# Kernel tuning notes

Measured on AMD Instinct MI355X. Metric: run time of the kernel, lower is better.

Reference implementation:

```python
import jax, jax.numpy as jnp
import numpy as np

BETA = 1.0
ALPHA = 0.5
M, D, B = 65536, 256, 512


def setup_inputs() -> dict:
    key = jax.random.key(0)
    k1, k2, k3 = jax.random.split(key, 3)
    v = jax.random.normal(k1, (B, D), dtype=jnp.float32)
    mask = jax.random.uniform(k2, (B, D), dtype=jnp.float32)
    memories = jax.random.normal(k3, (M, D), dtype=jnp.float32)
    return {"v": v, "mask": mask, "memories": memories}


def reference(v, mask, memories):
    # logits[m, b] = -beta/2 * ||memories[m] - v[b]||^2
    # expanded via ||a-b||^2 = ||a||^2 - 2 a.b + ||b||^2 (same math, no [M,D,B] tensor)
    mem_sq = jnp.sum(memories * memories, axis=1, keepdims=True)      # [M, 1]
    v_sq = jnp.sum(v * v, axis=1)[None, :]                            # [1, B]
    cross = jnp.einsum('md,bd->mb', memories, v)                      # [M, B]
    logits = -0.5 * BETA * (mem_sq - 2.0 * cross + v_sq)              # [M, B]
    # w = exp(logits) / sum_m exp(logits): stable softmax over memories
    w = jax.nn.softmax(logits, axis=0)                                # [M, B]
    # update[b, d] = sum_m w[m,b] * (memories[m,d] - v[b,d])
    #            = (w^T @ memories)[b,d] - v[b,d]
    update = jnp.einsum('mb,md->bd', w, memories) - v                 # [B, D]
    out = v + ALPHA * update * mask                                   # [B, D]
    return out
```

## Files before the change

kernel.cpp:

```cpp
#include <hip/hip_runtime.h>
#include <hip/hip_bf16.h>


#define D_DIM 256
#define B_DIM 512
#define M_TOT 65536
#define NSPLIT 64
#define CHUNK 64
#define NCHUNK 16

typedef __attribute__((ext_vector_type(4))) float f32x4;
typedef __attribute__((ext_vector_type(8))) short s16x8;
typedef __attribute__((ext_vector_type(2))) unsigned int u32x2;
typedef __attribute__((ext_vector_type(4))) unsigned int u32x4;

__device__ __forceinline__ unsigned short bf16rn(float f) {
  unsigned x = __builtin_bit_cast(unsigned, f);
  x += 0x7fffu + ((x >> 16) & 1u);
  return (unsigned short)(x >> 16);
}
__device__ __forceinline__ unsigned pk2(float a, float b) {
  return (unsigned)bf16rn(a) | ((unsigned)bf16rn(b) << 16);
}
__device__ __forceinline__ float bf2f(unsigned short u) {
  return __builtin_bit_cast(float, ((unsigned)u) << 16);
}

#define TSWZ(d) ((((d) ^ ((d) >> 3)) & 7) << 4)

__global__ __launch_bounds__(512) void k_prep(const float* __restrict__ memg,
                                              const float* __restrict__ v,
                                              unsigned short* __restrict__ memA,
                                              unsigned short* __restrict__ vbf,
                                              float* __restrict__ msq) {
  const int wg = (int)blockIdx.x;
  const int tid = (int)threadIdx.x;
  const int w = tid >> 6, lane = tid & 63;
  if (wg < 256) {
    size_t m0 = (size_t)wg * 256 + w * 32;
#pragma unroll 4
    for (int i = 0; i < 32; ++i) {
      size_t m = m0 + i;
      f32x4 f = *reinterpret_cast<const f32x4*>(memg + m * 256 + lane * 4);
      u32x2 p;
      p[0] = pk2(f[0], f[1]);
      p[1] = pk2(f[2], f[3]);
      *reinterpret_cast<u32x2*>(memA + m * 256 + lane * 4) = p;
      float sq = f[0] * f[0] + f[1] * f[1] + f[2] * f[2] + f[3] * f[3];
#pragma unroll
      for (int s2 = 32; s2; s2 >>= 1) sq += __shfl_xor(sq, s2);
      if (lane == 0) msq[m] = sq;
    }
  } else {
    size_t base = (size_t)(wg - 256) * 8192 + (size_t)tid * 16;
#pragma unroll
    for (int i = 0; i < 4; ++i) {
      f32x4 f = *reinterpret_cast<const f32x4*>(v + base + i * 4);
      u32x2 p;
      p[0] = pk2(f[0], f[1]);
      p[1] = pk2(f[2], f[3]);
      *reinterpret_cast<u32x2*>(vbf + base + i * 4) = p;
    }
  }
}

__global__ __launch_bounds__(512, 2) void k_stage1(
    const unsigned short* __restrict__ memA, const unsigned short* __restrict__ vbf,
    const float* __restrict__ msq, unsigned short* __restrict__ part_o,
    float* __restrict__ part_m, float* __restrict__ part_l) {
  __shared__ __align__(16) char lds[98304];
  char* const Ab0 = lds;
  char* const Ab1 = lds + 32768;
  char* const Tb = lds + 65536;

  const int tid = (int)threadIdx.x;
  const int w = tid >> 6;
  const int lane = tid & 63;
  const int g = lane >> 4;
  const int c = lane & 15;

  const int bid = (int)blockIdx.x;
  const int swz = (bid & 7) * 32 + (bid >> 3);
  const int s = swz >> 2;
  const int btile = swz & 3;
  const int mbase = s * 1024;
  const int bw = btile * 128 + w * 16;

  const char* memAc = (const char*)memA;
  const int mrow = w * 2 + (lane >> 5);
  const int dbyte = ((lane & 31) * 16) ^ ((mrow & 7) << 4);
  const size_t a_src0 = ((size_t)mbase + (size_t)mrow) * 512 + (size_t)dbyte;

#define STAGE(bufp, t)                                                          \
  do {                                                                          \
    _Pragma("unroll") for (int i_ = 0; i_ < 4; ++i_) {                          \
      __builtin_amdgcn_global_load_lds(                                         \
          (const __attribute__((address_space(1))) void*)(memAc + a_src0 +      \
              (size_t)(t) * 32768 + (size_t)i_ * 8192),                         \
          (__attribute__((address_space(3))) void*)((bufp) + i_ * 8192 + w * 1024), \
          16, 0, 0);                                                            \
    }                                                                           \
  } while (0)

  f32x4 acc[16];
#pragma unroll
  for (int n = 0; n < 16; ++n) acc[n] = (f32x4)0.0f;
  float rm = -__builtin_inff(), rs = 0.f;

  s16x8 vreg[8];

  STAGE(Ab0, 0);
#pragma unroll
  for (int k = 0; k < 8; ++k)
    vreg[k] = *reinterpret_cast<const s16x8*>(vbf + (size_t)(bw + c) * 256 + k * 32 + g * 8);

  asm volatile("s_waitcnt vmcnt(0)" ::: "memory");
  __builtin_amdgcn_s_barrier();
  asm volatile("" ::: "memory");

  const int db = tid & 31;
  const int mb = tid >> 5;
  const int d0 = db * 8, mm0 = mb * 4;

  for (int t = 0; t < NCHUNK; ++t) {
    char* Abc = (t & 1) ? Ab1 : Ab0;
    char* Abn = (t & 1) ? Ab0 : Ab1;
    if (t < NCHUNK - 1) STAGE(Abn, t + 1);

    {
      u32x4 r0 = *reinterpret_cast<const u32x4*>(Abc + (((mm0 + 0) * 512 + d0 * 2) ^ (((mm0 + 0) & 7) << 4)));
      u32x4 r1 = *reinterpret_cast<const u32x4*>(Abc + (((mm0 + 1) * 512 + d0 * 2) ^ (((mm0 + 1) & 7) << 4)));
      u32x4 r2 = *reinterpret_cast<const u32x4*>(Abc + (((mm0 + 2) * 512 + d0 * 2) ^ (((mm0 + 2) & 7) << 4)));
      u32x4 r3 = *reinterpret_cast<const u32x4*>(Abc + (((mm0 + 3) * 512 + d0 * 2) ^ (((mm0 + 3) & 7) << 4)));
#pragma unroll
      for (int dd = 0; dd < 8; ++dd) {
        int sh = (dd & 1) * 16;
        unsigned h0 = (r0[dd >> 1] >> sh) & 0xffffu;
        unsigned h1 = (r1[dd >> 1] >> sh) & 0xffffu;
        unsigned h2 = (r2[dd >> 1] >> sh) & 0xffffu;
        unsigned h3 = (r3[dd >> 1] >> sh) & 0xffffu;
        u32x2 pw;
        pw[0] = h0 | (h1 << 16);
        pw[1] = h2 | (h3 << 16);
        int d = d0 + dd;
        *reinterpret_cast<u32x2*>(Tb + ((d * 128 + mm0 * 2) ^ TSWZ(d))) = pw;
      }
    }
    asm volatile("s_waitcnt lgkmcnt(0)" ::: "memory");
    __builtin_amdgcn_s_barrier();
    asm volatile("" ::: "memory");

    const int mc = mbase + t * 64;
    f32x4 S[4];
#pragma unroll
    for (int rf = 0; rf < 4; ++rf) S[rf] = (f32x4)0.0f;
#pragma unroll
    for (int k = 0; k < 8; ++k) {
#pragma unroll
      for (int rf = 0; rf < 4; ++rf) {
        s16x8 a = *reinterpret_cast<const s16x8*>(
            Abc + (((rf * 16 + c) * 512 + k * 64 + g * 16) ^ ((c & 7) << 4)));
        S[rf] = __builtin_amdgcn_mfma_f32_16x16x32_bf16(a, vreg[k], S[rf], 0, 0, 0);
      }
    }
#pragma unroll
    for (int rf = 0; rf < 4; ++rf) {
      f32x4 q = *reinterpret_cast<const f32x4*>(msq + mc + rf * 16 + g * 4);
#pragma unroll
      for (int r = 0; r < 4; ++r) S[rf][r] -= 0.5f * q[r];
    }
    float mx = -__builtin_inff();
#pragma unroll
    for (int rf = 0; rf < 4; ++rf)
#pragma unroll
      for (int r = 0; r < 4; ++r) mx = fmaxf(mx, S[rf][r]);
    mx = fmaxf(mx, __shfl_xor(mx, 16));
    mx = fmaxf(mx, __shfl_xor(mx, 32));
    float nm = fmaxf(rm, mx);
    float al = __expf(rm - nm);
    float ls = 0.f;
#pragma unroll
    for (int rf = 0; rf < 4; ++rf)
#pragma unroll
      for (int r = 0; r < 4; ++r) {
        float p = __expf(S[rf][r] - nm);
        S[rf][r] = p;
        ls += p;
      }
    ls += __shfl_xor(ls, 16);
    ls += __shfl_xor(ls, 32);
    rs = rs * al + ls;
    rm = nm;
    f32x4 alv;
#pragma unroll
    for (int r = 0; r < 4; ++r) alv[r] = __shfl(al, 4 * g + r);
#pragma unroll
    for (int n = 0; n < 16; ++n) acc[n] *= alv;

#pragma unroll
    for (int kk = 0; kk < 2; ++kk) {
      unsigned q00 = pk2(S[2 * kk][0], S[2 * kk][1]);
      unsigned q01 = pk2(S[2 * kk][2], S[2 * kk][3]);
      unsigned q10 = pk2(S[2 * kk + 1][0], S[2 * kk + 1][1]);
      unsigned q11 = pk2(S[2 * kk + 1][2], S[2 * kk + 1][3]);
      int srcA = ((lane & 16) >> 3) * 16 + c;
      int srcB = srcA + 16;
      unsigned a0 = (unsigned)__shfl((int)q00, srcA);
      unsigned b0 = (unsigned)__shfl((int)q10, srcA);
      unsigned a1 = (unsigned)__shfl((int)q01, srcA);
      unsigned b1 = (unsigned)__shfl((int)q11, srcA);
      unsigned a2 = (unsigned)__shfl((int)q00, srcB);
      unsigned b2 = (unsigned)__shfl((int)q10, srcB);
      unsigned a3 = (unsigned)__shfl((int)q01, srcB);
      unsigned b3 = (unsigned)__shfl((int)q11, srcB);
      bool hi = lane >= 32;
      u32x4 wv;
      wv[0] = hi ? b0 : a0;
      wv[1] = hi ? b1 : a1;
      wv[2] = hi ? b2 : a2;
      wv[3] = hi ? b3 : a3;
      s16x8 pa = __builtin_bit_cast(s16x8, wv);
#pragma unroll
      for (int n = 0; n < 16; ++n) {
        int d = n * 16 + c;
        s16x8 bm = *reinterpret_cast<const s16x8*>(Tb + ((d * 128 + kk * 64 + g * 16) ^ TSWZ(d)));
        acc[n] = __builtin_amdgcn_mfma_f32_16x16x32_bf16(pa, bm, acc[n], 0, 0, 0);
      }
    }

    asm volatile("s_waitcnt vmcnt(0) lgkmcnt(0)" ::: "memory");
    __builtin_amdgcn_s_barrier();
    asm volatile("" ::: "memory");
  }

  if (lane < 16) {
    int b = bw + lane;
    part_m[(size_t)b * NSPLIT + s] = rm;
    part_l[(size_t)b * NSPLIT + s] = rs;
  }

  {
    char* ep = lds;
    const int base_w = w * 8448;
#pragma unroll
    for (int n = 0; n < 16; ++n) {
#pragma unroll
      for (int r = 0; r < 4; ++r) {
        *reinterpret_cast<unsigned short*>(ep + base_w + (4 * g + r) * 528 + (n * 16 + c) * 2) =
            bf16rn(acc[n][r]);
      }
    }
    asm volatile("s_waitcnt lgkmcnt(0)" ::: "memory");
    __builtin_amdgcn_s_barrier();
    asm volatile("" ::: "memory");
#pragma unroll
    for (int j = 0; j < 8; ++j) {
      int u = j * 512 + tid;
      int wb = u >> 5;
      int d8 = u & 31;
      u32x4 val = *reinterpret_cast<const u32x4*>(ep + (wb >> 4) * 8448 + (wb & 15) * 528 + d8 * 16);
      *reinterpret_cast<u32x4*>(part_o +
          ((size_t)s * 512 + btile * 128 + wb) * 256 + d8 * 8) = val;
    }
  }
#undef STAGE
}

__global__ __launch_bounds__(64) void k_scale(const float* __restrict__ part_m,
                                              const float* __restrict__ part_l,
                                              float* __restrict__ scale) {
  int b = blockIdx.x, t = threadIdx.x;
  float m = part_m[(size_t)b * NSPLIT + t];
  float l = part_l[(size_t)b * NSPLIT + t];
  float M = m;
#pragma unroll
  for (int s2 = 32; s2; s2 >>= 1) M = fmaxf(M, __shfl_xor(M, s2));
  float e = __expf(m - M);
  float z = e * l;
#pragma unroll
  for (int s2 = 32; s2; s2 >>= 1) z += __shfl_xor(z, s2);
  scale[(size_t)b * NSPLIT + t] = e / z;
}

__global__ __launch_bounds__(256) void k_out(const unsigned short* __restrict__ part_o,
                                             const float* __restrict__ scale,
                                             const float* __restrict__ v,
                                             const float* __restrict__ mask,
                                             float* __restrict__ out) {
  int b = blockIdx.x, d = threadIdx.x;
  __shared__ float sc[NSPLIT];
  if (d < NSPLIT) sc[d] = scale[(size_t)b * NSPLIT + d];
  __syncthreads();
  float a = 0.f;
  const unsigned short* po = part_o + (size_t)b * 256 + d;
#pragma unroll 8
  for (int gi = 0; gi < NSPLIT; ++gi)
    a = fmaf(sc[gi], bf2f(po[(size_t)gi * 131072]), a);
  size_t idx = (size_t)b * 256 + d;
  float vv = v[idx], mm = mask[idx];
  out[idx] = vv + 0.5f * (a - vv) * mm;
}

extern "C" void kernel_launch(void* const* d_in, const int* in_sizes, int n_in,
                              void* d_out, int out_size, void* d_ws, size_t ws_size,
                              hipStream_t stream) {
  const float* v = (const float*)d_in[0];
  const float* mask = (const float*)d_in[1];
  const float* memg = (const float*)d_in[2];
  float* out = (float*)d_out;

  char* ws = (char*)d_ws;
  const size_t SZ_PO = (size_t)NSPLIT * B_DIM * D_DIM * 2;
  const size_t SZ_MA = (size_t)M_TOT * D_DIM * 2;
  const size_t SZ_MS = (size_t)M_TOT * 4;
  const size_t SZ_VB = (size_t)B_DIM * D_DIM * 2;
  const size_t SZ_ST = (size_t)B_DIM * NSPLIT * 4;
  unsigned short* part_o = (unsigned short*)ws;
  unsigned short* memA = (unsigned short*)(ws + SZ_PO);
  float* msq = (float*)(ws + SZ_PO + SZ_MA);
  unsigned short* vbf = (unsigned short*)(ws + SZ_PO + SZ_MA + SZ_MS);
  float* part_m = (float*)(ws + SZ_PO + SZ_MA + SZ_MS + SZ_VB);
  float* part_l = (float*)(ws + SZ_PO + SZ_MA + SZ_MS + SZ_VB + SZ_ST);
  float* scale = (float*)(ws + SZ_PO + SZ_MA + SZ_MS + SZ_VB + 2 * SZ_ST);

  k_prep<<<dim3(272), dim3(512), 0, stream>>>(memg, v, memA, vbf, msq);
  k_stage1<<<dim3(256), dim3(512), 0, stream>>>(memA, vbf, msq, part_o, part_m, part_l);
  k_scale<<<dim3(B_DIM), dim3(64), 0, stream>>>(part_m, part_l, scale);
  k_out<<<dim3(B_DIM), dim3(256), 0, stream>>>(part_o, scale, v, mask, out);
}
```

Measured before the change: 98.74 us.

## Process two batch tiles per wave, lazy softmax rescale, fuse scale into output kernel

Each wave now handles 32 batch columns with two accumulator sets, so every staged memory tile feeds twice as many MFMAs. To keep the grid at 256 blocks, the memory split count is doubled and chunks per block halved. Online-softmax rescaling of the accumulators is skipped unless the running max rises by more than 8, and the PV MFMA operand order is swapped. s_setprio hints are added around the MFMA loops, and the k_scale kernel is folded into k_out to remove one launch. In exchange, register pressure doubles for accumulators and the partial-output buffer that k_out must reduce gets twice as large.

```diff
diff --git a/kernel.cpp b/kernel.cpp
--- a/kernel.cpp
+++ b/kernel.cpp
@@ -5,9 +5,9 @@
 #define D_DIM 256
 #define B_DIM 512
 #define M_TOT 65536
-#define NSPLIT 64
+#define NSPLIT 128
 #define CHUNK 64
-#define NCHUNK 16
+#define NCHUNK 8
 
 typedef __attribute__((ext_vector_type(4))) float f32x4;
 typedef __attribute__((ext_vector_type(8))) short s16x8;
@@ -64,6 +64,58 @@
   }
 }
 
+#define SOFTMAX_UPD(S_, rm_, rs_, acc_)                                        \
+  {                                                                            \
+    float mx = S_[0][0];                                                       \
+    _Pragma("unroll") for (int rf_ = 0; rf_ < 4; ++rf_)                        \
+        _Pragma("unroll") for (int r_ = 0; r_ < 4; ++r_)                       \
+            mx = fmaxf(mx, S_[rf_][r_]);                                       \
+    mx = fmaxf(mx, __shfl_xor(mx, 16));                                        \
+    mx = fmaxf(mx, __shfl_xor(mx, 32));                                        \
+    if (!__all(mx <= rm_ + 8.0f)) {                                            \
+      float nm = fmaxf(rm_, mx);                                               \
+      float al = __expf(rm_ - nm);                                             \
+      rm_ = nm;                                                                \
+      rs_ *= al;                                                               \
+      _Pragma("unroll") for (int n_ = 0; n_ < 16; ++n_) acc_[n_] = acc_[n_] * al; \
+    }                                                                          \
+    float ls = 0.f;                                                            \
+    _Pragma("unroll") for (int rf_ = 0; rf_ < 4; ++rf_)                        \
+        _Pragma("unroll") for (int r_ = 0; r_ < 4; ++r_) {                     \
+      float p_ = __expf(S_[rf_][r_] - rm_);                                    \
+      S_[rf_][r_] = p_;                                                        \
+      ls += p_;                                                                \
+    }                                                                          \
+    ls += __shfl_xor(ls, 16);                                                  \
+    ls += __shfl_xor(ls, 32);                                                  \
+    rs_ += ls;                                                                 \
+  }
+
+#define MAKE_PA(S_, kk_, pa_)                                                  \
+  {                                                                            \
+    unsigned q00 = pk2(S_[2 * kk_][0], S_[2 * kk_][1]);                        \
+    unsigned q01 = pk2(S_[2 * kk_][2], S_[2 * kk_][3]);                        \
+    unsigned q10 = pk2(S_[2 * kk_ + 1][0], S_[2 * kk_ + 1][1]);                \
+    unsigned q11 = pk2(S_[2 * kk_ + 1][2], S_[2 * kk_ + 1][3]);                \
+    int srcA = ((lane & 16) >> 3) * 16 + c;                                    \
+    int srcB = srcA + 16;                                                      \
+    unsigned a0 = (unsigned)__shfl((int)q00, srcA);                            \
+    unsigned b0 = (unsigned)__shfl((int)q10, srcA);                            \
+    unsigned a1 = (unsigned)__shfl((int)q01, srcA);                            \
+    unsigned b1 = (unsigned)__shfl((int)q11, srcA);                            \
+    unsigned a2 = (unsigned)__shfl((int)q00, srcB);                            \
+    unsigned b2 = (unsigned)__shfl((int)q10, srcB);                            \
+    unsigned a3 = (unsigned)__shfl((int)q01, srcB);                            \
+    unsigned b3 = (unsigned)__shfl((int)q11, srcB);                            \
+    bool hi = lane >= 32;                                                      \
+    u32x4 wv;                                                                  \
+    wv[0] = hi ? b0 : a0;                                                      \
+    wv[1] = hi ? b1 : a1;                                                      \
+    wv[2] = hi ? b2 : a2;                                                      \
+    wv[3] = hi ? b3 : a3;                                                      \
+    pa_ = __builtin_bit_cast(s16x8, wv);                                       \
+  }
+
 __global__ __launch_bounds__(512, 2) void k_stage1(
     const unsigned short* __restrict__ memA, const unsigned short* __restrict__ vbf,
     const float* __restrict__ msq, unsigned short* __restrict__ part_o,
@@ -81,15 +133,15 @@
 
   const int bid = (int)blockIdx.x;
   const int swz = (bid & 7) * 32 + (bid >> 3);
-  const int s = swz >> 2;
-  const int btile = swz & 3;
-  const int mbase = s * 1024;
-  const int bw = btile * 128 + w * 16;
+  const int s = swz >> 1;
+  const int btile = swz & 1;
+  const int mbase = s * 512;
+  const int bw = btile * 256 + w * 32;
 
   const char* memAc = (const char*)memA;
   const int mrow = w * 2 + (lane >> 5);
-  const int dbyte = ((lane & 31) * 16) ^ ((mrow & 7) << 4);
-  const size_t a_src0 = ((size_t)mbase + (size_t)mrow) * 512 + (size_t)dbyte;
+  const size_t a_src0 = ((size_t)mbase + (size_t)mrow) * 512 +
+                        (size_t)(((lane & 31) * 16) ^ ((mrow & 7) << 4));
 
 #define STAGE(bufp, t)                                                          \
   do {                                                                          \
@@ -102,17 +154,20 @@
     }                                                                           \
   } while (0)
 
-  f32x4 acc[16];
-#pragma unroll
-  for (int n = 0; n < 16; ++n) acc[n] = (f32x4)0.0f;
-  float rm = -__builtin_inff(), rs = 0.f;
-
-  s16x8 vreg[8];
+  f32x4 acc0[16], acc1[16];
+#pragma unroll
+  for (int n = 0; n < 16; ++n) { acc0[n] = (f32x4)0.0f; acc1[n] = (f32x4)0.0f; }
+  float rm0 = -__builtin_inff(), rs0 = 0.f;
+  float rm1 = -__builtin_inff(), rs1 = 0.f;
+
+  s16x8 vr0[8], vr1[8];
 
   STAGE(Ab0, 0);
 #pragma unroll
-  for (int k = 0; k < 8; ++k)
-    vreg[k] = *reinterpret_cast<const s16x8*>(vbf + (size_t)(bw + c) * 256 + k * 32 + g * 8);
+  for (int k = 0; k < 8; ++k) {
+    vr0[k] = *reinterpret_cast<const s16x8*>(vbf + (size_t)(bw + c) * 256 + k * 32 + g * 8);
+    vr1[k] = *reinterpret_cast<const s16x8*>(vbf + (size_t)(bw + 16 + c) * 256 + k * 32 + g * 8);
+  }
 
   asm volatile("s_waitcnt vmcnt(0)" ::: "memory");
   __builtin_amdgcn_s_barrier();
@@ -151,81 +206,46 @@
     asm volatile("" ::: "memory");
 
     const int mc = mbase + t * 64;
-    f32x4 S[4];
-#pragma unroll
-    for (int rf = 0; rf < 4; ++rf) S[rf] = (f32x4)0.0f;
+
+    f32x4 S0[4], S1[4];
+#pragma unroll
+    for (int rf = 0; rf < 4; ++rf) { S0[rf] = (f32x4)0.0f; S1[rf] = (f32x4)0.0f; }
+    __builtin_amdgcn_s_setprio(1);
 #pragma unroll
     for (int k = 0; k < 8; ++k) {
 #pragma unroll
       for (int rf = 0; rf < 4; ++rf) {
         s16x8 a = *reinterpret_cast<const s16x8*>(
             Abc + (((rf * 16 + c) * 512 + k * 64 + g * 16) ^ ((c & 7) << 4)));
-        S[rf] = __builtin_amdgcn_mfma_f32_16x16x32_bf16(a, vreg[k], S[rf], 0, 0, 0);
+        S0[rf] = __builtin_amdgcn_mfma_f32_16x16x32_bf16(a, vr0[k], S0[rf], 0, 0, 0);
+        S1[rf] = __builtin_amdgcn_mfma_f32_16x16x32_bf16(a, vr1[k], S1[rf], 0, 0, 0);
       }
     }
+    __builtin_amdgcn_s_setprio(0);
 #pragma unroll
     for (int rf = 0; rf < 4; ++rf) {
       f32x4 q = *reinterpret_cast<const f32x4*>(msq + mc + rf * 16 + g * 4);
 #pragma unroll
-      for (int r = 0; r < 4; ++r) S[rf][r] -= 0.5f * q[r];
-    }
-    float mx = -__builtin_inff();
-#pragma unroll
-    for (int rf = 0; rf < 4; ++rf)
-#pragma unroll
-      for (int r = 0; r < 4; ++r) mx = fmaxf(mx, S[rf][r]);
-    mx = fmaxf(mx, __shfl_xor(mx, 16));
-    mx = fmaxf(mx, __shfl_xor(mx, 32));
-    float nm = fmaxf(rm, mx);
-    float al = __expf(rm - nm);
-    float ls = 0.f;
-#pragma unroll
-    for (int rf = 0; rf < 4; ++rf)
-#pragma unroll
-      for (int r = 0; r < 4; ++r) {
-        float p = __expf(S[rf][r] - nm);
-        S[rf][r] = p;
-        ls += p;
-      }
-    ls += __shfl_xor(ls, 16);
-    ls += __shfl_xor(ls, 32);
-    rs = rs * al + ls;
-    rm = nm;
-    f32x4 alv;
-#pragma unroll
-    for (int r = 0; r < 4; ++r) alv[r] = __shfl(al, 4 * g + r);
-#pragma unroll
-    for (int n = 0; n < 16; ++n) acc[n] *= alv;
+      for (int r = 0; r < 4; ++r) { S0[rf][r] -= 0.5f * q[r]; S1[rf][r] -= 0.5f * q[r]; }
+    }
+
+    SOFTMAX_UPD(S0, rm0, rs0, acc0);
+    SOFTMAX_UPD(S1, rm1, rs1, acc1);
 
 #pragma unroll
     for (int kk = 0; kk < 2; ++kk) {
-      unsigned q00 = pk2(S[2 * kk][0], S[2 * kk][1]);
-      unsigned q01 = pk2(S[2 * kk][2], S[2 * kk][3]);
-      unsigned q10 = pk2(S[2 * kk + 1][0], S[2 * kk + 1][1]);
-      unsigned q11 = pk2(S[2 * kk + 1][2], S[2 * kk + 1][3]);
-      int srcA = ((lane & 16) >> 3) * 16 + c;
-      int srcB = srcA + 16;
-      unsigned a0 = (unsigned)__shfl((int)q00, srcA);
-      unsigned b0 = (unsigned)__shfl((int)q10, srcA);
-      unsigned a1 = (unsigned)__shfl((int)q01, srcA);
-      unsigned b1 = (unsigned)__shfl((int)q11, srcA);
-      unsigned a2 = (unsigned)__shfl((int)q00, srcB);
-      unsigned b2 = (unsigned)__shfl((int)q10, srcB);
-      unsigned a3 = (unsigned)__shfl((int)q01, srcB);
-      unsigned b3 = (unsigned)__shfl((int)q11, srcB);
-      bool hi = lane >= 32;
-      u32x4 wv;
-      wv[0] = hi ? b0 : a0;
-      wv[1] = hi ? b1 : a1;
-      wv[2] = hi ? b2 : a2;
-      wv[3] = hi ? b3 : a3;
-      s16x8 pa = __builtin_bit_cast(s16x8, wv);
+      s16x8 pa0, pa1;
+      MAKE_PA(S0, kk, pa0);
+      MAKE_PA(S1, kk, pa1);
+      __builtin_amdgcn_s_setprio(1);
 #pragma unroll
       for (int n = 0; n < 16; ++n) {
         int d = n * 16 + c;
         s16x8 bm = *reinterpret_cast<const s16x8*>(Tb + ((d * 128 + kk * 64 + g * 16) ^ TSWZ(d)));
-        acc[n] = __builtin_amdgcn_mfma_f32_16x16x32_bf16(pa, bm, acc[n], 0, 0, 0);
+        acc0[n] = __builtin_amdgcn_mfma_f32_16x16x32_bf16(bm, pa0, acc0[n], 0, 0, 0);
+        acc1[n] = __builtin_amdgcn_mfma_f32_16x16x32_bf16(bm, pa1, acc1[n], 0, 0, 0);
       }
+      __builtin_amdgcn_s_setprio(0);
     }
 
     asm volatile("s_waitcnt vmcnt(0) lgkmcnt(0)" ::: "memory");
@@ -233,72 +253,77 @@
     asm volatile("" ::: "memory");
   }
 
-  if (lane < 16) {
-    int b = bw + lane;
-    part_m[(size_t)b * NSPLIT + s] = rm;
-    part_l[(size_t)b * NSPLIT + s] = rs;
+  if (g == 0) {
+    int b0s = bw + c;
+    part_m[(size_t)b0s * NSPLIT + s] = rm0;
+    part_l[(size_t)b0s * NSPLIT + s] = rs0;
+    part_m[(size_t)(b0s + 16) * NSPLIT + s] = rm1;
+    part_l[(size_t)(b0s + 16) * NSPLIT + s] = rs1;
   }
 
   {
     char* ep = lds;
-    const int base_w = w * 8448;
-#pragma unroll
-    for (int n = 0; n < 16; ++n) {
-#pragma unroll
-      for (int r = 0; r < 4; ++r) {
-        *reinterpret_cast<unsigned short*>(ep + base_w + (4 * g + r) * 528 + (n * 16 + c) * 2) =
-            bf16rn(acc[n][r]);
+#pragma unroll
+    for (int cf = 0; cf < 2; ++cf) {
+      __syncthreads();
+#pragma unroll
+      for (int n = 0; n < 16; ++n) {
+        u32x2 pw;
+        if (cf == 0) { pw[0] = pk2(acc0[n][0], acc0[n][1]); pw[1] = pk2(acc0[n][2], acc0[n][3]); }
+        else         { pw[0] = pk2(acc1[n][0], acc1[n][1]); pw[1] = pk2(acc1[n][2], acc1[n][3]); }
+        *reinterpret_cast<u32x2*>(ep + w * 8448 + c * 528 + (n * 16 + 4 * g) * 2) = pw;
       }
-    }
-    asm volatile("s_waitcnt lgkmcnt(0)" ::: "memory");
-    __builtin_amdgcn_s_barrier();
-    asm volatile("" ::: "memory");
-#pragma unroll
-    for (int j = 0; j < 8; ++j) {
-      int u = j * 512 + tid;
-      int wb = u >> 5;
-      int d8 = u & 31;
-      u32x4 val = *reinterpret_cast<const u32x4*>(ep + (wb >> 4) * 8448 + (wb & 15) * 528 + d8 * 16);
-      *reinterpret_cast<u32x4*>(part_o +
-          ((size_t)s * 512 + btile * 128 + wb) * 256 + d8 * 8) = val;
+      __syncthreads();
+      int row = tid >> 2, q = tid & 3;
+      size_t bglob = (size_t)btile * 256 + (size_t)(row >> 4) * 32 + (size_t)cf * 16 + (row & 15);
+      char* dst = (char*)part_o + ((size_t)s * 512 + bglob) * 512 + q * 128;
+      const char* srcp = ep + (row >> 4) * 8448 + (row & 15) * 528 + q * 128;
+#pragma unroll
+      for (int i = 0; i < 8; ++i)
+        *reinterpret_cast<u32x4*>(dst + i * 16) = *reinterpret_cast<const u32x4*>(srcp + i * 16);
     }
   }
 #undef STAGE
 }
 
-__global__ __launch_bounds__(64) void k_scale(const float* __restrict__ part_m,
-                                              const float* __restrict__ part_l,
-                                              float* __restrict__ scale) {
-  int b = blockIdx.x, t = threadIdx.x;
-  float m = part_m[(size_t)b * NSPLIT + t];
-  float l = part_l[(size_t)b * NSPLIT + t];
-  float M = m;
-#pragma unroll
-  for (int s2 = 32; s2; s2 >>= 1) M = fmaxf(M, __shfl_xor(M, s2));
-  float e = __expf(m - M);
-  float z = e * l;
-#pragma unroll
-  for (int s2 = 32; s2; s2 >>= 1) z += __shfl_xor(z, s2);
-  scale[(size_t)b * NSPLIT + t] = e / z;
-}
-
 __global__ __launch_bounds__(256) void k_out(const unsigned short* __restrict__ part_o,
-                                             const float* __restrict__ scale,
+                                             const float* __restrict__ part_m,
+                                             const float* __restrict__ part_l,
                                              const float* __restrict__ v,
                                              const float* __restrict__ mask,
                                              float* __restrict__ out) {
-  int b = blockIdx.x, d = threadIdx.x;
+  int b = blockIdx.x, t = threadIdx.x;
   __shared__ float sc[NSPLIT];
-  if (d < NSPLIT) sc[d] = scale[(size_t)b * NSPLIT + d];
+  __shared__ float red[8];
+  float m = -__builtin_inff(), l = 0.f;
+  if (t < NSPLIT) {
+    m = part_m[(size_t)b * NSPLIT + t];
+    l = part_l[(size_t)b * NSPLIT + t];
+  }
+  float mm = m;
+#pragma unroll
+  for (int s2 = 32; s2; s2 >>= 1) mm = fmaxf(mm, __shfl_xor(mm, s2));
+  if ((t & 63) == 0) red[t >> 6] = mm;
   __syncthreads();
+  float M = fmaxf(red[0], red[1]);
+  float e = (t < NSPLIT) ? __expf(m - M) : 0.f;
+  float z = e * l;
+#pragma unroll
+  for (int s2 = 32; s2; s2 >>= 1) z += __shfl_xor(z, s2);
+  if ((t & 63) == 0) red[4 + (t >> 6)] = z;
+  __syncthreads();
+  float Z = red[4] + red[5];
+  if (t < NSPLIT) sc[t] = e / Z;
+  __syncthreads();
+
   float a = 0.f;
-  const unsigned short* po = part_o + (size_t)b * 256 + d;
+  const unsigned short* po = part_o + (size_t)b * 256 + t;
 #pragma unroll 8
   for (int gi = 0; gi < NSPLIT; ++gi)
     a = fmaf(sc[gi], bf2f(po[(size_t)gi * 131072]), a);
-  size_t idx = (size_t)b * 256 + d;
-  float vv = v[idx], mm = mask[idx];
-  out[idx] = vv + 0.5f * (a - vv) * mm;
+  size_t idx = (size_t)b * 256 + t;
+  float vv = v[idx], mk = mask[idx];
+  out[idx] = vv + 0.5f * (a - vv) * mk;
 }
 
 extern "C" void kernel_launch(void* const* d_in, const int* in_sizes, int n_in,
@@ -321,10 +346,8 @@
   unsigned short* vbf = (unsigned short*)(ws + SZ_PO + SZ_MA + SZ_MS);
   float* part_m = (float*)(ws + SZ_PO + SZ_MA + SZ_MS + SZ_VB);
   float* part_l = (float*)(ws + SZ_PO + SZ_MA + SZ_MS + SZ_VB + SZ_ST);
-  float* scale = (float*)(ws + SZ_PO + SZ_MA + SZ_MS + SZ_VB + 2 * SZ_ST);
 
   k_prep<<<dim3(272), dim3(512), 0, stream>>>(memg, v, memA, vbf, msq);
   k_stage1<<<dim3(256), dim3(512), 0, stream>>>(memA, vbf, msq, part_o, part_m, part_l);
-  k_scale<<<dim3(B_DIM), dim3(64), 0, stream>>>(part_m, part_l, scale);
-  k_out<<<dim3(B_DIM), dim3(256), 0, stream>>>(part_o, scale, v, mask, out);
-}
+  k_out<<<dim3(B_DIM), dim3(256), 0, stream>>>(part_o, part_m, part_l, v, mask, out);
+}
```

Result: slower. 253.9 us (+157.2%).

## Rework flash-style stage1 with 32x32 MFMA, more splits, lazy rescale

Applied to the files above, without the earlier changes.

The main kernel now uses 256-thread blocks with 32x32x16 bf16 MFMAs in place of 16x16x32, 32-row memory chunks, and twice as many M splits (128). This raises the block count and reduces LDS per block. The online-softmax rescale is skipped unless the running max grows by more than a threshold, and s_setprio is raised around the MFMA sections. Partial outputs are written directly from registers in a d-blocked layout, and the reduce kernels are rewritten to match, with vectorized loads in k_out. The costs are twice the partial-output traffic and a larger reduction in k_out.

```diff
diff --git a/kernel.cpp b/kernel.cpp
--- a/kernel.cpp
+++ b/kernel.cpp
@@ -2,14 +2,11 @@
 #include <hip/hip_bf16.h>
 
 
-#define D_DIM 256
-#define B_DIM 512
-#define M_TOT 65536
-#define NSPLIT 64
-#define CHUNK 64
+#define NSPLIT 128
 #define NCHUNK 16
 
 typedef __attribute__((ext_vector_type(4))) float f32x4;
+typedef __attribute__((ext_vector_type(16))) float f32x16;
 typedef __attribute__((ext_vector_type(8))) short s16x8;
 typedef __attribute__((ext_vector_type(2))) unsigned int u32x2;
 typedef __attribute__((ext_vector_type(4))) unsigned int u32x4;
@@ -64,74 +61,81 @@
   }
 }
 
-__global__ __launch_bounds__(512, 2) void k_stage1(
+__global__ __launch_bounds__(256) void k_stage1(
     const unsigned short* __restrict__ memA, const unsigned short* __restrict__ vbf,
     const float* __restrict__ msq, unsigned short* __restrict__ part_o,
     float* __restrict__ part_m, float* __restrict__ part_l) {
-  __shared__ __align__(16) char lds[98304];
+  __shared__ __align__(16) char lds[65536];
   char* const Ab0 = lds;
-  char* const Ab1 = lds + 32768;
-  char* const Tb = lds + 65536;
+  char* const Ab1 = lds + 16384;
+  char* const Tb = lds + 32768;
 
   const int tid = (int)threadIdx.x;
   const int w = tid >> 6;
   const int lane = tid & 63;
-  const int g = lane >> 4;
-  const int c = lane & 15;
+  const int hi = lane >> 5;
+  const int c5 = lane & 31;
 
   const int bid = (int)blockIdx.x;
-  const int swz = (bid & 7) * 32 + (bid >> 3);
+  const int swz = (bid & 7) * 64 + (bid >> 3);
   const int s = swz >> 2;
   const int btile = swz & 3;
-  const int mbase = s * 1024;
-  const int bw = btile * 128 + w * 16;
-
-  const char* memAc = (const char*)memA;
-  const int mrow = w * 2 + (lane >> 5);
-  const int dbyte = ((lane & 31) * 16) ^ ((mrow & 7) << 4);
-  const size_t a_src0 = ((size_t)mbase + (size_t)mrow) * 512 + (size_t)dbyte;
-
-#define STAGE(bufp, t)                                                          \
-  do {                                                                          \
-    _Pragma("unroll") for (int i_ = 0; i_ < 4; ++i_) {                          \
-      __builtin_amdgcn_global_load_lds(                                         \
-          (const __attribute__((address_space(1))) void*)(memAc + a_src0 +      \
-              (size_t)(t) * 32768 + (size_t)i_ * 8192),                         \
-          (__attribute__((address_space(3))) void*)((bufp) + i_ * 8192 + w * 1024), \
-          16, 0, 0);                                                            \
-    }                                                                           \
+  const int bw = btile * 128 + w * 32;
+  const int b = bw + c5;
+
+  const char* Ac = (const char*)memA;
+  const size_t qsrc = (size_t)s * 262144 + (size_t)(tid >> 5) * 512 +
+                      (size_t)(((tid & 31) ^ (tid >> 5)) * 16);
+
+#define STAGE(bufp, t_)                                                          \
+  do {                                                                           \
+    _Pragma("unroll") for (int i_ = 0; i_ < 4; ++i_) {                           \
+      __builtin_amdgcn_global_load_lds(                                          \
+          (const __attribute__((address_space(1))) void*)(Ac + qsrc +            \
+              (size_t)(t_) * 16384 + (size_t)i_ * 4096),                         \
+          (__attribute__((address_space(3))) void*)((bufp) + w * 1024 + i_ * 4096), \
+          16, 0, 0);                                                             \
+    }                                                                            \
   } while (0)
 
-  f32x4 acc[16];
-#pragma unroll
-  for (int n = 0; n < 16; ++n) acc[n] = (f32x4)0.0f;
+  f32x16 acc[8];
+#pragma unroll
+  for (int n = 0; n < 8; ++n) acc[n] = (f32x16)0.0f;
   float rm = -__builtin_inff(), rs = 0.f;
 
-  s16x8 vreg[8];
-
+  s16x8 vr[16];
   STAGE(Ab0, 0);
 #pragma unroll
-  for (int k = 0; k < 8; ++k)
-    vreg[k] = *reinterpret_cast<const s16x8*>(vbf + (size_t)(bw + c) * 256 + k * 32 + g * 8);
+  for (int k = 0; k < 16; ++k)
+    vr[k] = *reinterpret_cast<const s16x8*>(vbf + (size_t)b * 256 + k * 16 + hi * 8);
 
   asm volatile("s_waitcnt vmcnt(0)" ::: "memory");
   __builtin_amdgcn_s_barrier();
   asm volatile("" ::: "memory");
 
-  const int db = tid & 31;
-  const int mb = tid >> 5;
-  const int d0 = db * 8, mm0 = mb * 4;
+  const int mbt = tid >> 5;
+  const int dbt = tid & 31;
 
   for (int t = 0; t < NCHUNK; ++t) {
     char* Abc = (t & 1) ? Ab1 : Ab0;
     char* Abn = (t & 1) ? Ab0 : Ab1;
     if (t < NCHUNK - 1) STAGE(Abn, t + 1);
 
+    const char* qb = Abc + c5 * 512;
+    f32x16 S = (f32x16)0.0f;
+    __builtin_amdgcn_s_setprio(1);
+#pragma unroll
+    for (int k = 0; k < 16; ++k) {
+      s16x8 a = *reinterpret_cast<const s16x8*>(qb + ((k * 32 + hi * 16) ^ ((c5 & 7) << 4)));
+      S = __builtin_amdgcn_mfma_f32_32x32x16_bf16(a, vr[k], S, 0, 0, 0);
+    }
+    __builtin_amdgcn_s_setprio(0);
+
     {
-      u32x4 r0 = *reinterpret_cast<const u32x4*>(Abc + (((mm0 + 0) * 512 + d0 * 2) ^ (((mm0 + 0) & 7) << 4)));
-      u32x4 r1 = *reinterpret_cast<const u32x4*>(Abc + (((mm0 + 1) * 512 + d0 * 2) ^ (((mm0 + 1) & 7) << 4)));
-      u32x4 r2 = *reinterpret_cast<const u32x4*>(Abc + (((mm0 + 2) * 512 + d0 * 2) ^ (((mm0 + 2) & 7) << 4)));
-      u32x4 r3 = *reinterpret_cast<const u32x4*>(Abc + (((mm0 + 3) * 512 + d0 * 2) ^ (((mm0 + 3) & 7) << 4)));
+      u32x4 r0 = *reinterpret_cast<const u32x4*>(Abc + (mbt * 4 + 0) * 512 + ((dbt * 16) ^ (((mbt * 4 + 0) & 7) << 4)));
+      u32x4 r1 = *reinterpret_cast<const u32x4*>(Abc + (mbt * 4 + 1) * 512 + ((dbt * 16) ^ (((mbt * 4 + 1) & 7) << 4)));
+      u32x4 r2 = *reinterpret_cast<const u32x4*>(Abc + (mbt * 4 + 2) * 512 + ((dbt * 16) ^ (((mbt * 4 + 2) & 7) << 4)));
+      u32x4 r3 = *reinterpret_cast<const u32x4*>(Abc + (mbt * 4 + 3) * 512 + ((dbt * 16) ^ (((mbt * 4 + 3) & 7) << 4)));
 #pragma unroll
       for (int dd = 0; dd < 8; ++dd) {
         int sh = (dd & 1) * 16;
@@ -142,163 +146,148 @@
         u32x2 pw;
         pw[0] = h0 | (h1 << 16);
         pw[1] = h2 | (h3 << 16);
-        int d = d0 + dd;
-        *reinterpret_cast<u32x2*>(Tb + ((d * 128 + mm0 * 2) ^ TSWZ(d))) = pw;
+        int d = dbt * 8 + dd;
+        *reinterpret_cast<u32x2*>(Tb + ((d * 128 + mbt * 8) ^ TSWZ(d))) = pw;
       }
     }
     asm volatile("s_waitcnt lgkmcnt(0)" ::: "memory");
     __builtin_amdgcn_s_barrier();
     asm volatile("" ::: "memory");
 
-    const int mc = mbase + t * 64;
-    f32x4 S[4];
-#pragma unroll
-    for (int rf = 0; rf < 4; ++rf) S[rf] = (f32x4)0.0f;
-#pragma unroll
-    for (int k = 0; k < 8; ++k) {
-#pragma unroll
-      for (int rf = 0; rf < 4; ++rf) {
-        s16x8 a = *reinterpret_cast<const s16x8*>(
-            Abc + (((rf * 16 + c) * 512 + k * 64 + g * 16) ^ ((c & 7) << 4)));
-        S[rf] = __builtin_amdgcn_mfma_f32_16x16x32_bf16(a, vreg[k], S[rf], 0, 0, 0);
+    const int mc = s * 512 + t * 32;
+#pragma unroll
+    for (int q = 0; q < 4; ++q) {
+      f32x4 qq = *reinterpret_cast<const f32x4*>(msq + mc + 8 * q + 4 * hi);
+#pragma unroll
+      for (int r = 0; r < 4; ++r) S[4 * q + r] -= 0.5f * qq[r];
+    }
+
+    float mx = S[0];
+#pragma unroll
+    for (int i = 1; i < 16; ++i) mx = fmaxf(mx, S[i]);
+    mx = fmaxf(mx, __shfl_xor(mx, 32));
+    if (!__all(mx <= rm + 8.0f)) {
+      float nm = fmaxf(rm, mx);
+      float al = __expf(rm - nm);
+      rm = nm;
+      rs *= al;
+#pragma unroll
+      for (int n = 0; n < 8; ++n) acc[n] *= al;
+    }
+    float ls = 0.f;
+#pragma unroll
+    for (int i = 0; i < 16; ++i) {
+      float p = __expf(S[i] - rm);
+      S[i] = p;
+      ls += p;
+    }
+    ls += __shfl_xor(ls, 32);
+    rs += ls;
+
+    unsigned pkd[8];
+#pragma unroll
+    for (int p = 0; p < 8; ++p) pkd[p] = pk2(S[2 * p], S[2 * p + 1]);
+    s16x8 pb0, pb1;
+#pragma unroll
+    for (int kk = 0; kk < 2; ++kk) {
+      u32x4 wv;
+#pragma unroll
+      for (int i = 0; i < 4; ++i) {
+        const int src = (i >> 1) * 32 + c5;
+        unsigned lo = (unsigned)__shfl((int)pkd[(i & 1) + 4 * kk], src);
+        unsigned hv = (unsigned)__shfl((int)pkd[(i & 1) + 4 * kk + 2], src);
+        wv[i] = hi ? hv : lo;
       }
-    }
-#pragma unroll
-    for (int rf = 0; rf < 4; ++rf) {
-      f32x4 q = *reinterpret_cast<const f32x4*>(msq + mc + rf * 16 + g * 4);
-#pragma unroll
-      for (int r = 0; r < 4; ++r) S[rf][r] -= 0.5f * q[r];
-    }
-    float mx = -__builtin_inff();
-#pragma unroll
-    for (int rf = 0; rf < 4; ++rf)
-#pragma unroll
-      for (int r = 0; r < 4; ++r) mx = fmaxf(mx, S[rf][r]);
-    mx = fmaxf(mx, __shfl_xor(mx, 16));
-    mx = fmaxf(mx, __shfl_xor(mx, 32));
-    float nm = fmaxf(rm, mx);
-    float al = __expf(rm - nm);
-    float ls = 0.f;
-#pragma unroll
-    for (int rf = 0; rf < 4; ++rf)
-#pragma unroll
-      for (int r = 0; r < 4; ++r) {
-        float p = __expf(S[rf][r] - nm);
-        S[rf][r] = p;
-        ls += p;
-      }
-    ls += __shfl_xor(ls, 16);
-    ls += __shfl_xor(ls, 32);
-    rs = rs * al + ls;
-    rm = nm;
-    f32x4 alv;
-#pragma unroll
-    for (int r = 0; r < 4; ++r) alv[r] = __shfl(al, 4 * g + r);
-#pragma unroll
-    for (int n = 0; n < 16; ++n) acc[n] *= alv;
-
-#pragma unroll
-    for (int kk = 0; kk < 2; ++kk) {
-      unsigned q00 = pk2(S[2 * kk][0], S[2 * kk][1]);
-      unsigned q01 = pk2(S[2 * kk][2], S[2 * kk][3]);
-      unsigned q10 = pk2(S[2 * kk + 1][0], S[2 * kk + 1][1]);
-      unsigned q11 = pk2(S[2 * kk + 1][2], S[2 * kk + 1][3]);
-      int srcA = ((lane & 16) >> 3) * 16 + c;
-      int srcB = srcA + 16;
-      unsigned a0 = (unsigned)__shfl((int)q00, srcA);
-      unsigned b0 = (unsigned)__shfl((int)q10, srcA);
-      unsigned a1 = (unsigned)__shfl((int)q01, srcA);
-      unsigned b1 = (unsigned)__shfl((int)q11, srcA);
-      unsigned a2 = (unsigned)__shfl((int)q00, srcB);
-      unsigned b2 = (unsigned)__shfl((int)q10, srcB);
-      unsigned a3 = (unsigned)__shfl((int)q01, srcB);
-      unsigned b3 = (unsigned)__shfl((int)q11, srcB);
-      bool hi = lane >= 32;
-      u32x4 wv;
-      wv[0] = hi ? b0 : a0;
-      wv[1] = hi ? b1 : a1;
-      wv[2] = hi ? b2 : a2;
-      wv[3] = hi ? b3 : a3;
-      s16x8 pa = __builtin_bit_cast(s16x8, wv);
-#pragma unroll
-      for (int n = 0; n < 16; ++n) {
-        int d = n * 16 + c;
-        s16x8 bm = *reinterpret_cast<const s16x8*>(Tb + ((d * 128 + kk * 64 + g * 16) ^ TSWZ(d)));
-        acc[n] = __builtin_amdgcn_mfma_f32_16x16x32_bf16(pa, bm, acc[n], 0, 0, 0);
-      }
-    }
-
-    asm volatile("s_waitcnt vmcnt(0) lgkmcnt(0)" ::: "memory");
+      if (kk == 0) pb0 = __builtin_bit_cast(s16x8, wv);
+      else         pb1 = __builtin_bit_cast(s16x8, wv);
+    }
+
+    __builtin_amdgcn_s_setprio(1);
+#pragma unroll
+    for (int n = 0; n < 8; ++n) {
+      const int d = n * 32 + c5;
+      s16x8 bm0 = *reinterpret_cast<const s16x8*>(Tb + ((d * 128 + hi * 16) ^ TSWZ(d)));
+      s16x8 bm1 = *reinterpret_cast<const s16x8*>(Tb + ((d * 128 + 32 + hi * 16) ^ TSWZ(d)));
+      acc[n] = __builtin_amdgcn_mfma_f32_32x32x16_bf16(bm0, pb0, acc[n], 0, 0, 0);
+      acc[n] = __builtin_amdgcn_mfma_f32_32x32x16_bf16(bm1, pb1, acc[n], 0, 0, 0);
+    }
+    __builtin_amdgcn_s_setprio(0);
+
+    asm volatile("s_waitcnt vmcnt(0)" ::: "memory");
     __builtin_amdgcn_s_barrier();
     asm volatile("" ::: "memory");
   }
 
-  if (lane < 16) {
-    int b = bw + lane;
-    part_m[(size_t)b * NSPLIT + s] = rm;
-    part_l[(size_t)b * NSPLIT + s] = rs;
-  }
-
-  {
-    char* ep = lds;
-    const int base_w = w * 8448;
-#pragma unroll
-    for (int n = 0; n < 16; ++n) {
-#pragma unroll
-      for (int r = 0; r < 4; ++r) {
-        *reinterpret_cast<unsigned short*>(ep + base_w + (4 * g + r) * 528 + (n * 16 + c) * 2) =
-            bf16rn(acc[n][r]);
-      }
-    }
-    asm volatile("s_waitcnt lgkmcnt(0)" ::: "memory");
-    __builtin_amdgcn_s_barrier();
-    asm volatile("" ::: "memory");
-#pragma unroll
-    for (int j = 0; j < 8; ++j) {
-      int u = j * 512 + tid;
-      int wb = u >> 5;
-      int d8 = u & 31;
-      u32x4 val = *reinterpret_cast<const u32x4*>(ep + (wb >> 4) * 8448 + (wb & 15) * 528 + d8 * 16);
-      *reinterpret_cast<u32x4*>(part_o +
-          ((size_t)s * 512 + btile * 128 + wb) * 256 + d8 * 8) = val;
+  if (hi == 0) {
+    part_m[(size_t)s * 512 + b] = rm;
+    part_l[(size_t)s * 512 + b] = rs;
+  }
+
+#pragma unroll
+  for (int n = 0; n < 8; ++n) {
+#pragma unroll
+    for (int q = 0; q < 4; ++q) {
+      u32x2 pw;
+      pw[0] = pk2(acc[n][4 * q + 0], acc[n][4 * q + 1]);
+      pw[1] = pk2(acc[n][4 * q + 2], acc[n][4 * q + 3]);
+      *reinterpret_cast<u32x2*>(part_o + (size_t)s * 131072 +
+                                (size_t)(n * 8 + 2 * q + hi) * 2048 + (size_t)b * 4) = pw;
     }
   }
 #undef STAGE
 }
 
-__global__ __launch_bounds__(64) void k_scale(const float* __restrict__ part_m,
-                                              const float* __restrict__ part_l,
-                                              float* __restrict__ scale) {
-  int b = blockIdx.x, t = threadIdx.x;
-  float m = part_m[(size_t)b * NSPLIT + t];
-  float l = part_l[(size_t)b * NSPLIT + t];
-  float M = m;
-#pragma unroll
-  for (int s2 = 32; s2; s2 >>= 1) M = fmaxf(M, __shfl_xor(M, s2));
+__global__ __launch_bounds__(128) void k_scale(const float* __restrict__ part_m,
+                                               const float* __restrict__ part_l,
+                                               float* __restrict__ scale) {
+  const int b = (int)blockIdx.x, t = (int)threadIdx.x;
+  const int wv = t >> 6;
+  __shared__ float red[4];
+  float m = part_m[(size_t)t * 512 + b];
+  float l = part_l[(size_t)t * 512 + b];
+  float mm = m;
+#pragma unroll
+  for (int s2 = 32; s2; s2 >>= 1) mm = fmaxf(mm, __shfl_xor(mm, s2));
+  if ((t & 63) == 0) red[wv] = mm;
+  __syncthreads();
+  float M = fmaxf(red[0], red[1]);
   float e = __expf(m - M);
   float z = e * l;
 #pragma unroll
   for (int s2 = 32; s2; s2 >>= 1) z += __shfl_xor(z, s2);
-  scale[(size_t)b * NSPLIT + t] = e / z;
-}
-
-__global__ __launch_bounds__(256) void k_out(const unsigned short* __restrict__ part_o,
+  if ((t & 63) == 0) red[2 + wv] = z;
+  __syncthreads();
+  float Z = red[2] + red[3];
+  scale[(size_t)t * 512 + b] = e / Z;
+}
+
+__global__ __launch_bounds__(128) void k_out(const unsigned short* __restrict__ part_o,
                                              const float* __restrict__ scale,
                                              const float* __restrict__ v,
                                              const float* __restrict__ mask,
                                              float* __restrict__ out) {
-  int b = blockIdx.x, d = threadIdx.x;
-  __shared__ float sc[NSPLIT];
-  if (d < NSPLIT) sc[d] = scale[(size_t)b * NSPLIT + d];
-  __syncthreads();
-  float a = 0.f;
-  const unsigned short* po = part_o + (size_t)b * 256 + d;
+  const int dblk = (int)blockIdx.x >> 2;
+  const int b = ((int)blockIdx.x & 3) * 128 + (int)threadIdx.x;
+  float a0 = 0.f, a1 = 0.f, a2 = 0.f, a3 = 0.f;
+  const unsigned short* po = part_o + (size_t)dblk * 2048 + (size_t)b * 4;
 #pragma unroll 8
-  for (int gi = 0; gi < NSPLIT; ++gi)
-    a = fmaf(sc[gi], bf2f(po[(size_t)gi * 131072]), a);
-  size_t idx = (size_t)b * 256 + d;
-  float vv = v[idx], mm = mask[idx];
-  out[idx] = vv + 0.5f * (a - vv) * mm;
+  for (int gi = 0; gi < NSPLIT; ++gi) {
+    u32x2 pw = *reinterpret_cast<const u32x2*>(po + (size_t)gi * 131072);
+    float sc = scale[(size_t)gi * 512 + b];
+    a0 = fmaf(sc, bf2f((unsigned short)pw[0]), a0);
+    a1 = fmaf(sc, bf2f((unsigned short)(pw[0] >> 16)), a1);
+    a2 = fmaf(sc, bf2f((unsigned short)pw[1]), a2);
+    a3 = fmaf(sc, bf2f((unsigned short)(pw[1] >> 16)), a3);
+  }
+  const size_t idx = (size_t)b * 256 + (size_t)dblk * 4;
+  f32x4 vv = *reinterpret_cast<const f32x4*>(v + idx);
+  f32x4 mk = *reinterpret_cast<const f32x4*>(mask + idx);
+  f32x4 o;
+  o[0] = vv[0] + 0.5f * (a0 - vv[0]) * mk[0];
+  o[1] = vv[1] + 0.5f * (a1 - vv[1]) * mk[1];
+  o[2] = vv[2] + 0.5f * (a2 - vv[2]) * mk[2];
+  o[3] = vv[3] + 0.5f * (a3 - vv[3]) * mk[3];
+  *reinterpret_cast<f32x4*>(out + idx) = o;
 }
 
 extern "C" void kernel_launch(void* const* d_in, const int* in_sizes, int n_in,
@@ -310,11 +299,11 @@
   float* out = (float*)d_out;
 
   char* ws = (char*)d_ws;
-  const size_t SZ_PO = (size_t)NSPLIT * B_DIM * D_DIM * 2;
-  const size_t SZ_MA = (size_t)M_TOT * D_DIM * 2;
-  const size_t SZ_MS = (size_t)M_TOT * 4;
-  const size_t SZ_VB = (size_t)B_DIM * D_DIM * 2;
-  const size_t SZ_ST = (size_t)B_DIM * NSPLIT * 4;
+  const size_t SZ_PO = (size_t)NSPLIT * 64 * 512 * 4 * 2;
+  const size_t SZ_MA = (size_t)65536 * 256 * 2;
+  const size_t SZ_MS = (size_t)65536 * 4;
+  const size_t SZ_VB = (size_t)512 * 256 * 2;
+  const size_t SZ_ST = (size_t)NSPLIT * 512 * 4;
   unsigned short* part_o = (unsigned short*)ws;
   unsigned short* memA = (unsigned short*)(ws + SZ_PO);
   float* msq = (float*)(ws + SZ_PO + SZ_MA);
@@ -324,7 +313,7 @@
   float* scale = (float*)(ws + SZ_PO + SZ_MA + SZ_MS + SZ_VB + 2 * SZ_ST);
 
   k_prep<<<dim3(272), dim3(512), 0, stream>>>(memg, v, memA, vbf, msq);
-  k_stage1<<<dim3(256), dim3(512), 0, stream>>>(memA, vbf, msq, part_o, part_m, part_l);
-  k_scale<<<dim3(B_DIM), dim3(64), 0, stream>>>(part_m, part_l, scale);
-  k_out<<<dim3(B_DIM), dim3(256), 0, stream>>>(part_o, scale, v, mask, out);
-}
+  k_stage1<<<dim3(512), dim3(256), 0, stream>>>(memA, vbf, msq, part_o, part_m, part_l);
+  k_scale<<<dim3(512), dim3(128), 0, stream>>>(part_m, part_l, scale);
+  k_out<<<dim3(256), dim3(128), 0, stream>>>(part_o, scale, v, mask, out);
+}
```

Result: slower. 144.8 us (+46.6%).
